# Performance work log

Measured on AMD Instinct MI355X. Metric: run time of the kernel, lower is better.

The kernel has to match this reference:

```python
import math
import jax, jax.numpy as jnp
import numpy as np

N_HEAD = 16

def setup_inputs() -> dict:
    key = jax.random.key(0)
    ks = jax.random.split(key, 7)
    B, T, C = 4, 2048, 1024
    QL, KVL = 256, 256
    s = 0.02
    return {
        "x":     jax.random.normal(ks[0], (B, T, C), jnp.float32),
        "W_dq":  jax.random.normal(ks[1], (QL, C), jnp.float32) * s,
        "W_uq":  jax.random.normal(ks[2], (C, QL), jnp.float32) * s,
        "W_dkv": jax.random.normal(ks[3], (KVL, C), jnp.float32) * s,
        "W_uk":  jax.random.normal(ks[4], (C, KVL), jnp.float32) * s,
        "W_uv":  jax.random.normal(ks[5], (C, KVL), jnp.float32) * s,
        "W_o":   jax.random.normal(ks[6], (C, C), jnp.float32) * s,
    }

def reference(x, W_dq, W_uq, W_dkv, W_uk, W_uv, W_o):
    B, T, C = x.shape
    nh = N_HEAD
    hs = C // nh
    kvl = W_dkv.shape[0]
    # Absorbed projection matrices (training path: recomputed each call)
    # k_eff: (nh, hs, kvl); v_eff: (nh, kvl, hs)
    k_eff = (W_dq.T @ W_uq.T @ W_uk).reshape(nh, hs, kvl)
    v_eff = (W_uv.T @ W_o.T).reshape(kvl, nh, hs).transpose(1, 0, 2)
    # Latent KV cache: (B, T, kvl)
    c_kv = x @ W_dkv.T
    # Queries: (B, nh, T, hs)
    q = (x @ W_dq.T @ W_uq.T).reshape(B, T, nh, hs).transpose(0, 2, 1, 3)
    # Scores: q @ k_eff @ c_kv^T / sqrt(hs) -> (B, nh, T, T)
    q_lat = jnp.einsum('bhtd,hdl->bhtl', q, k_eff)
    attn = jnp.einsum('bhtl,bsl->bhts', q_lat, c_kv) / math.sqrt(hs)
    causal_mask = jnp.triu(jnp.ones((T, T), bool), k=1)
    attn = jnp.where(causal_mask[None, None], -jnp.inf, attn)
    attn = jax.nn.softmax(attn, axis=-1)  # dropout p=0 -> identity
    # Output: attn @ c_kv @ v_eff -> (B, T, C)
    ctx = jnp.einsum('bhts,bsl->bhtl', attn, c_kv)
    y = jnp.einsum('bhtl,hld->bhtd', ctx, v_eff).transpose(0, 2, 1, 3).reshape(B, T, C)
    return (y, c_kv)
```

## Files before the change

### kernel.cpp

```cpp
#include <hip/hip_runtime.h>

typedef unsigned short u16;
typedef __attribute__((ext_vector_type(8))) short short8;
typedef __attribute__((ext_vector_type(4))) float f32x4;

#define MFMA_BF16 __builtin_amdgcn_mfma_f32_16x16x32_bf16

__device__ __forceinline__ u16 f2bf(float f){
  unsigned int u = __builtin_bit_cast(unsigned int, f);
  u += 0x7fffu + ((u >> 16) & 1u);
  return (u16)(u >> 16);
}

__device__ __forceinline__ void gld16(const void* g, void* l){
  __builtin_amdgcn_global_load_lds(
      (const __attribute__((address_space(1))) unsigned int*)g,
      (__attribute__((address_space(3))) unsigned int*)l, 16, 0, 0);
}

__global__ void k_transpose4(const float* __restrict__ s0, float* __restrict__ d0,
                             const float* __restrict__ s1, float* __restrict__ d1,
                             const float* __restrict__ s2, float* __restrict__ d2,
                             const float* __restrict__ s3, float* __restrict__ d3)
{
  __shared__ float tile[32][33];
  int z = blockIdx.z;
  const float* src = z == 0 ? s0 : z == 1 ? s1 : z == 2 ? s2 : s3;
  float* dst       = z == 0 ? d0 : z == 1 ? d1 : z == 2 ? d2 : d3;
  int rows = z == 0 ? 256 : 1024, cols = z == 0 ? 1024 : 256;
  int c0 = blockIdx.x * 32, r0 = blockIdx.y * 32;
  if (c0 >= cols || r0 >= rows) return;
  int tx = threadIdx.x, ty = threadIdx.y;
#pragma unroll
  for (int i = 0; i < 4; ++i){
    int r = ty + i * 8;
    tile[r][tx] = src[(long)(r0 + r) * cols + c0 + tx];
  }
  __syncthreads();
#pragma unroll
  for (int i = 0; i < 4; ++i){
    int r = ty + i * 8;
    dst[(long)(c0 + r) * rows + r0 + tx] = tile[tx][r];
  }
}

__global__ __launch_bounds__(256)
void k_gemm_nt(const float* __restrict__ A, const float* __restrict__ B,
               float* __restrict__ Cf, u16* __restrict__ Cb,
               int M, int N, int K, int lda, int ldb, int ldc,
               long sA, long sB, long sC, float scale)
{
  A += (long)blockIdx.z * sA; B += (long)blockIdx.z * sB;
  if (Cf) Cf += (long)blockIdx.z * sC;
  if (Cb) Cb += (long)blockIdx.z * sC;
  const int n0 = blockIdx.x * 64, m0 = blockIdx.y * 64;
  const int tid = threadIdx.x;
  const int wave = tid >> 6, lane = tid & 63, quad = lane >> 4, l16 = lane & 15;
  __shared__ u16 As[64 * 40];
  __shared__ u16 Bs[64 * 40];
  f32x4 acc[4];
#pragma unroll
  for (int n = 0; n < 4; ++n) acc[n] = (f32x4){0.f, 0.f, 0.f, 0.f};

  const int lr = tid >> 2;
  const int lc = (tid & 3) * 8;
  for (int k0 = 0; k0 < K; k0 += 32){
    {
      const float* pa = &A[(long)(m0 + lr) * lda + k0 + lc];
      float4 a0 = *(const float4*)pa;
      float4 a1 = *(const float4*)(pa + 4);
      short8 pk;
      pk[0]=(short)f2bf(a0.x); pk[1]=(short)f2bf(a0.y); pk[2]=(short)f2bf(a0.z); pk[3]=(short)f2bf(a0.w);
      pk[4]=(short)f2bf(a1.x); pk[5]=(short)f2bf(a1.y); pk[6]=(short)f2bf(a1.z); pk[7]=(short)f2bf(a1.w);
      *(short8*)&As[lr * 40 + lc] = pk;
      const float* pb = &B[(long)(n0 + lr) * ldb + k0 + lc];
      float4 b0 = *(const float4*)pb;
      float4 b1 = *(const float4*)(pb + 4);
      short8 qk;
      qk[0]=(short)f2bf(b0.x); qk[1]=(short)f2bf(b0.y); qk[2]=(short)f2bf(b0.z); qk[3]=(short)f2bf(b0.w);
      qk[4]=(short)f2bf(b1.x); qk[5]=(short)f2bf(b1.y); qk[6]=(short)f2bf(b1.z); qk[7]=(short)f2bf(b1.w);
      *(short8*)&Bs[lr * 40 + lc] = qk;
    }
    __syncthreads();
    short8 a = *(const short8*)&As[(wave * 16 + l16) * 40 + quad * 8];
#pragma unroll
    for (int n = 0; n < 4; ++n){
      short8 b = *(const short8*)&Bs[(n * 16 + l16) * 40 + quad * 8];
      acc[n] = MFMA_BF16(a, b, acc[n], 0, 0, 0);
    }
    __syncthreads();
  }
#pragma unroll
  for (int n = 0; n < 4; ++n)
#pragma unroll
    for (int r = 0; r < 4; ++r){
      int row = m0 + wave * 16 + quad * 4 + r;
      int col = n0 + n * 16 + l16;
      float v = acc[n][r] * scale;
      if (Cf) Cf[(long)row * ldc + col] = v;
      if (Cb) Cb[(long)row * ldc + col] = f2bf(v);
    }
}

__global__ __launch_bounds__(256)
void k_proj(const float* __restrict__ x, const float* __restrict__ Wdq,
            const float* __restrict__ Wdkv, u16* __restrict__ xq,
            float* __restrict__ ckv_f, u16* __restrict__ ckv_bf, u16* __restrict__ ckvT)
{
  const bool is_kv = blockIdx.x >= 4;
  const float* B = is_kv ? Wdkv : Wdq;
  const int n0 = (blockIdx.x & 3) * 64, m0 = blockIdx.y * 64;
  const int tid = threadIdx.x;
  const int wave = tid >> 6, lane = tid & 63, quad = lane >> 4, l16 = lane & 15;
  __shared__ u16 As[64 * 40];
  __shared__ u16 Bs[64 * 40];
  f32x4 acc[4];
#pragma unroll
  for (int n = 0; n < 4; ++n) acc[n] = (f32x4){0.f, 0.f, 0.f, 0.f};

  const int lr = tid >> 2;
  const int lc = (tid & 3) * 8;
  for (int k0 = 0; k0 < 1024; k0 += 32){
    {
      const float* pa = &x[(long)(m0 + lr) * 1024 + k0 + lc];
      float4 a0 = *(const float4*)pa;
      float4 a1 = *(const float4*)(pa + 4);
      short8 pk;
      pk[0]=(short)f2bf(a0.x); pk[1]=(short)f2bf(a0.y); pk[2]=(short)f2bf(a0.z); pk[3]=(short)f2bf(a0.w);
      pk[4]=(short)f2bf(a1.x); pk[5]=(short)f2bf(a1.y); pk[6]=(short)f2bf(a1.z); pk[7]=(short)f2bf(a1.w);
      *(short8*)&As[lr * 40 + lc] = pk;
      const float* pb = &B[(long)(n0 + lr) * 1024 + k0 + lc];
      float4 b0 = *(const float4*)pb;
      float4 b1 = *(const float4*)(pb + 4);
      short8 qk;
      qk[0]=(short)f2bf(b0.x); qk[1]=(short)f2bf(b0.y); qk[2]=(short)f2bf(b0.z); qk[3]=(short)f2bf(b0.w);
      qk[4]=(short)f2bf(b1.x); qk[5]=(short)f2bf(b1.y); qk[6]=(short)f2bf(b1.z); qk[7]=(short)f2bf(b1.w);
      *(short8*)&Bs[lr * 40 + lc] = qk;
    }
    __syncthreads();
    short8 a = *(const short8*)&As[(wave * 16 + l16) * 40 + quad * 8];
#pragma unroll
    for (int n = 0; n < 4; ++n){
      short8 b = *(const short8*)&Bs[(n * 16 + l16) * 40 + quad * 8];
      acc[n] = MFMA_BF16(a, b, acc[n], 0, 0, 0);
    }
    __syncthreads();
  }
  if (!is_kv){
#pragma unroll
    for (int n = 0; n < 4; ++n)
#pragma unroll
      for (int r = 0; r < 4; ++r){
        int row = m0 + wave * 16 + quad * 4 + r;
        int col = n0 + n * 16 + l16;
        xq[(long)row * 256 + col] = f2bf(acc[n][r]);
      }
  } else {
    const int b = (m0 >> 11);
    const int t0 = (m0 & 2047) + wave * 16 + quad * 4;
#pragma unroll
    for (int n = 0; n < 4; ++n){
      int col = n0 + n * 16 + l16;
      u16 pk[4];
#pragma unroll
      for (int r = 0; r < 4; ++r){
        int row = m0 + wave * 16 + quad * 4 + r;
        float v = acc[n][r];
        ckv_f [(long)row * 256 + col] = v;
        ckv_bf[(long)row * 256 + col] = f2bf(v);
        pk[r] = f2bf(v);
      }
      *(uint2*)&ckvT[((long)b * 256 + col) * 2048 + t0] = *(uint2*)pk;
    }
  }
}

__global__ __launch_bounds__(256, 2)
void k_flash(const u16* __restrict__ xq, const u16* __restrict__ Pt,
             const u16* __restrict__ ckv_bf, const u16* __restrict__ ckvT,
             const u16* __restrict__ Vt, float* __restrict__ y)
{
  const int qt = 31 - blockIdx.x, h = blockIdx.y, b = blockIdx.z;
  const int tid = threadIdx.x;
  const int wg = tid >> 6, lane = tid & 63, quad = lane >> 4, l16 = lane & 15;

  __shared__ u16 X0[64 * 256];
  __shared__ u16 X1[256 * 64];

  const int trow = wg * 16 + l16;
  const long tglob = (long)b * 2048 + qt * 64;
  const int sw_t = trow & 7;

  const u16* ckv_b  = ckv_bf + (long)b * 2048 * 256;
  const u16* ckvT_b = ckvT   + (long)b * 256 * 2048;

  const u16* srcA[8]; const u16* srcB[8];
  {
    int l5 = lane >> 5, g32 = lane & 31;
#pragma unroll
    for (int j = 0; j < 8; ++j){
      int s = (wg * 8 + j) * 2 + l5;
      int g = g32 ^ (s & 7);
      srcA[j] = ckv_b + (long)s * 256 + g * 8;
    }
    int l3 = lane >> 3, g8 = lane & 7;
#pragma unroll
    for (int j = 0; j < 8; ++j){
      int l = (wg * 8 + j) * 8 + l3;
      int g = g8 ^ (l & 7);
      srcB[j] = ckvT_b + (long)l * 2048 + g * 8;
    }
  }

  short8 aS[8];
  {
    short8 bq[8];
    const u16* xr = xq + (tglob + trow) * 256;
#pragma unroll
    for (int ks = 0; ks < 8; ++ks)
      bq[ks] = *(const short8*)&xr[ks * 32 + quad * 8];
    const u16* pth = Pt + (long)h * 65536;
#pragma unroll
    for (int mb = 0; mb < 16; ++mb){
      f32x4 acc = (f32x4){0.f, 0.f, 0.f, 0.f};
#pragma unroll
      for (int ks = 0; ks < 8; ++ks){
        short8 pa = *(const short8*)&pth[(mb * 16 + l16) * 256 + ks * 32 + quad * 8];
        acc = MFMA_BF16(pa, bq[ks], acc, 0, 0, 0);
      }
#pragma unroll
      for (int r = 0; r < 4; ++r){
        int l = mb * 16 + quad * 4 + r;
        int cs = (((l >> 3) ^ (l16 & 7)) << 3) | (l & 7);
        X0[trow * 256 + cs] = f2bf(acc[r]);
      }
    }
  }
  __syncthreads();
#pragma unroll
  for (int ks = 0; ks < 8; ++ks){
    int gl = ks * 4 + quad;
    aS[ks] = *(const short8*)&X0[trow * 256 + ((gl ^ sw_t) << 3)];
  }

  float m_t = -1e30f, l_t = 0.f;
  f32x4 oacc[16];
#pragma unroll
  for (int n = 0; n < 16; ++n) oacc[n] = (f32x4){0.f, 0.f, 0.f, 0.f};

  for (int st = 0; st <= qt; ++st){
    __syncthreads();
#pragma unroll
    for (int j = 0; j < 8; ++j)
      gld16(srcA[j] + (long)st * 16384, &X0[(wg * 8 + j) * 512]);
#pragma unroll
    for (int j = 0; j < 8; ++j)
      gld16(srcB[j] + st * 64, &X1[(wg * 8 + j) * 512]);
    __syncthreads();

    f32x4 sacc[4];
#pragma unroll
    for (int mb = 0; mb < 4; ++mb) sacc[mb] = (f32x4){0.f, 0.f, 0.f, 0.f};
#pragma unroll
    for (int ks = 0; ks < 8; ++ks){
#pragma unroll
      for (int mb = 0; mb < 4; ++mb){
        int gl = ks * 4 + quad;
        short8 a = *(const short8*)&X0[(mb * 16 + l16) * 256 + ((gl ^ (l16 & 7)) << 3)];
        sacc[mb] = MFMA_BF16(a, aS[ks], sacc[mb], 0, 0, 0);
      }
    }
    if (st == qt){
      int t = qt * 64 + trow;
#pragma unroll
      for (int mb = 0; mb < 4; ++mb)
#pragma unroll
        for (int r = 0; r < 4; ++r)
          if (st * 64 + mb * 16 + quad * 4 + r > t) sacc[mb][r] = -1e30f;
    }

    float pm[4][4];
    {
      float rm = sacc[0][0];
#pragma unroll
      for (int mb = 0; mb < 4; ++mb)
#pragma unroll
        for (int r = 0; r < 4; ++r) rm = fmaxf(rm, sacc[mb][r]);
      rm = fmaxf(rm, __shfl_xor(rm, 16, 64));
      rm = fmaxf(rm, __shfl_xor(rm, 32, 64));
      float mnew = fmaxf(m_t, rm);
      float alpha = __expf(m_t - mnew);
      m_t = mnew;
      float rs = 0.f;
#pragma unroll
      for (int mb = 0; mb < 4; ++mb)
#pragma unroll
        for (int r = 0; r < 4; ++r){
          float pe = __expf(sacc[mb][r] - mnew);
          pm[mb][r] = pe;
          rs += pe;
        }
      rs += __shfl_xor(rs, 16, 64);
      rs += __shfl_xor(rs, 32, 64);
      l_t = l_t * alpha + rs;
#pragma unroll
      for (int r2 = 0; r2 < 4; ++r2){
        float ar = __shfl(alpha, quad * 4 + r2, 64);
#pragma unroll
        for (int n = 0; n < 16; ++n) oacc[n][r2] *= ar;
      }
    }
    __syncthreads();
#pragma unroll
    for (int mb = 0; mb < 4; ++mb)
#pragma unroll
      for (int r = 0; r < 4; ++r)
        X0[trow * 72 + mb * 16 + quad * 4 + r] = f2bf(pm[mb][r]);
    __syncthreads();

    {
      short8 a0 = *(const short8*)&X0[trow * 72 + quad * 8];
      short8 a1 = *(const short8*)&X0[trow * 72 + 32 + quad * 8];
#pragma unroll
      for (int n = 0; n < 16; ++n){
        int lr_ = n * 16 + l16;
        int swl = lr_ & 7;
        short8 b0 = *(const short8*)&X1[lr_ * 64 + ((quad ^ swl) << 3)];
        short8 b1 = *(const short8*)&X1[lr_ * 64 + (((4 + quad) ^ swl) << 3)];
        oacc[n] = MFMA_BF16(a0, b0, oacc[n], 0, 0, 0);
        oacc[n] = MFMA_BF16(a1, b1, oacc[n], 0, 0, 0);
      }
    }
  }

  __syncthreads();
  {
    float linv = 1.f / l_t;
#pragma unroll
    for (int r = 0; r < 4; ++r){
      float lr_ = __shfl(linv, quad * 4 + r, 64);
#pragma unroll
      for (int n = 0; n < 16; ++n) oacc[n][r] *= lr_;
    }
#pragma unroll
    for (int n = 0; n < 16; ++n)
#pragma unroll
      for (int r = 0; r < 4; ++r){
        int trw = wg * 16 + quad * 4 + r;
        int l = n * 16 + l16;
        int cs = (((l >> 3) ^ (trw & 7)) << 3) | (l & 7);
        X0[trw * 256 + cs] = f2bf(oacc[n][r]);
      }
  }
  __syncthreads();
  {
    const u16* vth = Vt + (long)h * 64 * 256;
    short8 ca[8];
#pragma unroll
    for (int ks = 0; ks < 8; ++ks){
      int gl = ks * 4 + quad;
      ca[ks] = *(const short8*)&X0[trow * 256 + ((gl ^ sw_t) << 3)];
    }
#pragma unroll
    for (int n = 0; n < 4; ++n){
      f32x4 acc = (f32x4){0.f, 0.f, 0.f, 0.f};
#pragma unroll
      for (int ks = 0; ks < 8; ++ks){
        short8 vb = *(const short8*)&vth[(n * 16 + l16) * 256 + ks * 32 + quad * 8];
        acc = MFMA_BF16(ca[ks], vb, acc, 0, 0, 0);
      }
#pragma unroll
      for (int r = 0; r < 4; ++r)
        y[(tglob + wg * 16 + quad * 4 + r) * 1024 + h * 64 + n * 16 + l16] = acc[r];
    }
  }
}

extern "C" void kernel_launch(void* const* d_in, const int* in_sizes, int n_in,
                              void* d_out, int out_size, void* d_ws, size_t ws_size,
                              hipStream_t stream)
{
  (void)in_sizes; (void)n_in; (void)out_size; (void)ws_size;
  const float* x    = (const float*)d_in[0];
  const float* Wdq  = (const float*)d_in[1];
  const float* Wuq  = (const float*)d_in[2];
  const float* Wdkv = (const float*)d_in[3];
  const float* Wuk  = (const float*)d_in[4];
  const float* Wuv  = (const float*)d_in[5];
  const float* Wo   = (const float*)d_in[6];

  float* y_out   = (float*)d_out;
  float* ckv_out = y_out + (size_t)4 * 2048 * 1024;

  char* base = (char*)d_ws;
  float* wdqT   = (float*)(base + 0);
  float* wuqT   = (float*)(base + 1048576);
  float* wukT   = (float*)(base + 2097152);
  float* wuvT   = (float*)(base + 3145728);
  u16*   ckvT   = (u16*)  (base + 0);
  float* t1T    = (float*)(base + 4194304);
  float* keffT  = (float*)(base + 4456448);
  u16*   pt     = (u16*)  (base + 5505024);
  u16*   vt     = (u16*)  (base + 7602176);
  u16*   xq     = (u16*)  (base + 8126464);
  u16*   ckv_bf = (u16*)  (base + 12320768);

  k_transpose4<<<dim3(32, 32, 4), dim3(32, 8), 0, stream>>>(
      Wdq, wdqT, Wuq, wuqT, Wuk, wukT, Wuv, wuvT);

  k_gemm_nt<<<dim3(4, 4, 1), 256, 0, stream>>>(wukT, wuqT, t1T, (u16*)0,
      256, 256, 1024, 1024, 1024, 256, 0, 0, 0, 1.f);
  k_gemm_nt<<<dim3(16, 4, 1), 256, 0, stream>>>(t1T, wdqT, keffT, (u16*)0,
      256, 1024, 256, 256, 256, 1024, 0, 0, 0, 1.f);
  k_gemm_nt<<<dim3(4, 4, 16), 256, 0, stream>>>(keffT, wuqT, (float*)0, pt,
      256, 256, 64, 1024, 1024, 256, 64, 64, 65536, 0.125f);
  k_gemm_nt<<<dim3(4, 16, 1), 256, 0, stream>>>(Wo, wuvT, (float*)0, vt,
      1024, 256, 1024, 1024, 1024, 256, 0, 0, 0, 1.f);

  k_proj<<<dim3(8, 128), 256, 0, stream>>>(x, Wdq, Wdkv, xq, ckv_out, ckv_bf, ckvT);

  k_flash<<<dim3(32, 16, 4), 256, 0, stream>>>(xq, pt, ckv_bf, ckvT, vt, y_out);
}
```

Baseline: 737.9 us.

## Use 128-row query tiles with 8 waves and per-wave P buffers in flash kernel

Each flash block now covers 128 query rows with 512 threads (8 waves), so every loaded 64-key tile of the latent KV is shared by twice as many rows, halving global/LDS load traffic per row. The probability tile is written to a per-wave LDS buffer, which removes two block-wide barriers per iteration. Softmax rescaling is skipped unless the running max rises by more than 8 (lazy rescale), and MFMA sections get raised wave priority. Waves whose rows lie entirely before a key tile skip its compute but still join the loads. The trade-offs are more registers and LDS per block, and some imbalance between waves near the causal diagonal.

Result: slower. 795.7 us (+7.8%).

```diff
diff --git a/kernel.cpp b/kernel.cpp
--- a/kernel.cpp
+++ b/kernel.cpp
@@ -175,40 +175,40 @@
   }
 }
 
-__global__ __launch_bounds__(256, 2)
+__global__ __launch_bounds__(512, 4)
 void k_flash(const u16* __restrict__ xq, const u16* __restrict__ Pt,
              const u16* __restrict__ ckv_bf, const u16* __restrict__ ckvT,
              const u16* __restrict__ Vt, float* __restrict__ y)
 {
-  const int qt = 31 - blockIdx.x, h = blockIdx.y, b = blockIdx.z;
+  const int qt = 15 - blockIdx.x, h = blockIdx.y, b = blockIdx.z;
   const int tid = threadIdx.x;
   const int wg = tid >> 6, lane = tid & 63, quad = lane >> 4, l16 = lane & 15;
 
-  __shared__ u16 X0[64 * 256];
-  __shared__ u16 X1[256 * 64];
+  __shared__ u16 LDS[40960];
+  u16* X0 = LDS;
+  u16* X1 = LDS + 16384;
+  u16* PW = LDS + 32768 + wg * 1024;
 
   const int trow = wg * 16 + l16;
-  const long tglob = (long)b * 2048 + qt * 64;
-  const int sw_t = trow & 7;
+  const int swr  = l16 & 7;
+  const long tglob = (long)b * 2048 + qt * 128;
 
   const u16* ckv_b  = ckv_bf + (long)b * 2048 * 256;
   const u16* ckvT_b = ckvT   + (long)b * 256 * 2048;
 
-  const u16* srcA[8]; const u16* srcB[8];
+  int offA[4], offB[4];
   {
     int l5 = lane >> 5, g32 = lane & 31;
 #pragma unroll
-    for (int j = 0; j < 8; ++j){
-      int s = (wg * 8 + j) * 2 + l5;
-      int g = g32 ^ (s & 7);
-      srcA[j] = ckv_b + (long)s * 256 + g * 8;
+    for (int j = 0; j < 4; ++j){
+      int s = (wg * 4 + j) * 2 + l5;
+      offA[j] = s * 256 + ((g32 ^ (s & 7)) * 8);
     }
     int l3 = lane >> 3, g8 = lane & 7;
 #pragma unroll
-    for (int j = 0; j < 8; ++j){
-      int l = (wg * 8 + j) * 8 + l3;
-      int g = g8 ^ (l & 7);
-      srcB[j] = ckvT_b + (long)l * 2048 + g * 8;
+    for (int j = 0; j < 4; ++j){
+      int l = (wg * 4 + j) * 8 + l3;
+      offB[j] = l * 2048 + ((g8 ^ (l & 7)) * 8);
     }
   }
 
@@ -231,8 +231,8 @@
 #pragma unroll
       for (int r = 0; r < 4; ++r){
         int l = mb * 16 + quad * 4 + r;
-        int cs = (((l >> 3) ^ (l16 & 7)) << 3) | (l & 7);
-        X0[trow * 256 + cs] = f2bf(acc[r]);
+        int cs = (((l >> 3) ^ swr) << 3) | (l & 7);
+        LDS[trow * 256 + cs] = f2bf(acc[r]);
       }
     }
   }
@@ -240,7 +240,7 @@
 #pragma unroll
   for (int ks = 0; ks < 8; ++ks){
     int gl = ks * 4 + quad;
-    aS[ks] = *(const short8*)&X0[trow * 256 + ((gl ^ sw_t) << 3)];
+    aS[ks] = *(const short8*)&LDS[trow * 256 + ((gl ^ swr) << 3)];
   }
 
   float m_t = -1e30f, l_t = 0.f;
@@ -248,61 +248,55 @@
 #pragma unroll
   for (int n = 0; n < 16; ++n) oacc[n] = (f32x4){0.f, 0.f, 0.f, 0.f};
 
-  for (int st = 0; st <= qt; ++st){
-    __syncthreads();
-#pragma unroll
-    for (int j = 0; j < 8; ++j)
-      gld16(srcA[j] + (long)st * 16384, &X0[(wg * 8 + j) * 512]);
-#pragma unroll
-    for (int j = 0; j < 8; ++j)
-      gld16(srcB[j] + st * 64, &X1[(wg * 8 + j) * 512]);
-    __syncthreads();
+  const int stmax = 2 * qt + 1;
+  const int tg = qt * 128 + trow;
+  for (int st = 0; st <= stmax; ++st){
+    __syncthreads();
+#pragma unroll
+    for (int j = 0; j < 4; ++j)
+      gld16(ckv_b + (long)st * 16384 + offA[j], &X0[(wg * 4 + j) * 512]);
+#pragma unroll
+    for (int j = 0; j < 4; ++j)
+      gld16(ckvT_b + st * 64 + offB[j], &X1[(wg * 4 + j) * 512]);
+    __syncthreads();
+
+    if (st * 64 > qt * 128 + wg * 16 + 15) continue;
 
     f32x4 sacc[4];
 #pragma unroll
     for (int mb = 0; mb < 4; ++mb) sacc[mb] = (f32x4){0.f, 0.f, 0.f, 0.f};
+    __builtin_amdgcn_s_setprio(1);
 #pragma unroll
     for (int ks = 0; ks < 8; ++ks){
+      int gl = ks * 4 + quad;
 #pragma unroll
       for (int mb = 0; mb < 4; ++mb){
-        int gl = ks * 4 + quad;
-        short8 a = *(const short8*)&X0[(mb * 16 + l16) * 256 + ((gl ^ (l16 & 7)) << 3)];
+        short8 a = *(const short8*)&X0[(mb * 16 + l16) * 256 + ((gl ^ swr) << 3)];
         sacc[mb] = MFMA_BF16(a, aS[ks], sacc[mb], 0, 0, 0);
       }
     }
-    if (st == qt){
-      int t = qt * 64 + trow;
+    __builtin_amdgcn_s_setprio(0);
+
+    if (st * 64 + 63 > tg){
 #pragma unroll
       for (int mb = 0; mb < 4; ++mb)
 #pragma unroll
         for (int r = 0; r < 4; ++r)
-          if (st * 64 + mb * 16 + quad * 4 + r > t) sacc[mb][r] = -1e30f;
-    }
-
-    float pm[4][4];
-    {
-      float rm = sacc[0][0];
-#pragma unroll
-      for (int mb = 0; mb < 4; ++mb)
-#pragma unroll
-        for (int r = 0; r < 4; ++r) rm = fmaxf(rm, sacc[mb][r]);
-      rm = fmaxf(rm, __shfl_xor(rm, 16, 64));
-      rm = fmaxf(rm, __shfl_xor(rm, 32, 64));
+          if (st * 64 + mb * 16 + quad * 4 + r > tg) sacc[mb][r] = -1e30f;
+    }
+
+    float rm = sacc[0][0];
+#pragma unroll
+    for (int mb = 0; mb < 4; ++mb)
+#pragma unroll
+      for (int r = 0; r < 4; ++r) rm = fmaxf(rm, sacc[mb][r]);
+    rm = fmaxf(rm, __shfl_xor(rm, 16, 64));
+    rm = fmaxf(rm, __shfl_xor(rm, 32, 64));
+    if (!__all(rm <= m_t + 8.f)){
       float mnew = fmaxf(m_t, rm);
       float alpha = __expf(m_t - mnew);
       m_t = mnew;
-      float rs = 0.f;
-#pragma unroll
-      for (int mb = 0; mb < 4; ++mb)
-#pragma unroll
-        for (int r = 0; r < 4; ++r){
-          float pe = __expf(sacc[mb][r] - mnew);
-          pm[mb][r] = pe;
-          rs += pe;
-        }
-      rs += __shfl_xor(rs, 16, 64);
-      rs += __shfl_xor(rs, 32, 64);
-      l_t = l_t * alpha + rs;
+      l_t *= alpha;
 #pragma unroll
       for (int r2 = 0; r2 < 4; ++r2){
         float ar = __shfl(alpha, quad * 4 + r2, 64);
@@ -310,27 +304,37 @@
         for (int n = 0; n < 16; ++n) oacc[n][r2] *= ar;
       }
     }
-    __syncthreads();
-#pragma unroll
-    for (int mb = 0; mb < 4; ++mb)
-#pragma unroll
-      for (int r = 0; r < 4; ++r)
-        X0[trow * 72 + mb * 16 + quad * 4 + r] = f2bf(pm[mb][r]);
-    __syncthreads();
-
-    {
-      short8 a0 = *(const short8*)&X0[trow * 72 + quad * 8];
-      short8 a1 = *(const short8*)&X0[trow * 72 + 32 + quad * 8];
-#pragma unroll
-      for (int n = 0; n < 16; ++n){
-        int lr_ = n * 16 + l16;
-        int swl = lr_ & 7;
-        short8 b0 = *(const short8*)&X1[lr_ * 64 + ((quad ^ swl) << 3)];
-        short8 b1 = *(const short8*)&X1[lr_ * 64 + (((4 + quad) ^ swl) << 3)];
-        oacc[n] = MFMA_BF16(a0, b0, oacc[n], 0, 0, 0);
-        oacc[n] = MFMA_BF16(a1, b1, oacc[n], 0, 0, 0);
-      }
-    }
+    float rs = 0.f;
+#pragma unroll
+    for (int mb = 0; mb < 4; ++mb){
+      float p0 = __expf(sacc[mb][0] - m_t);
+      float p1 = __expf(sacc[mb][1] - m_t);
+      float p2 = __expf(sacc[mb][2] - m_t);
+      float p3 = __expf(sacc[mb][3] - m_t);
+      rs += (p0 + p1) + (p2 + p3);
+      unsigned int w0 = (unsigned)f2bf(p0) | ((unsigned)f2bf(p1) << 16);
+      unsigned int w1 = (unsigned)f2bf(p2) | ((unsigned)f2bf(p3) << 16);
+      int pos = (2 * mb + (quad >> 1)) ^ swr;
+      uint2 w; w.x = w0; w.y = w1;
+      *(uint2*)&PW[l16 * 64 + pos * 8 + (quad & 1) * 4] = w;
+    }
+    rs += __shfl_xor(rs, 16, 64);
+    rs += __shfl_xor(rs, 32, 64);
+    l_t += rs;
+
+    short8 a0 = *(const short8*)&PW[l16 * 64 + ((quad ^ swr) << 3)];
+    short8 a1 = *(const short8*)&PW[l16 * 64 + (((4 + quad) ^ swr) << 3)];
+    __builtin_amdgcn_s_setprio(1);
+#pragma unroll
+    for (int n = 0; n < 16; ++n){
+      int lr_ = n * 16 + l16;
+      int swl = lr_ & 7;
+      short8 b0 = *(const short8*)&X1[lr_ * 64 + ((quad ^ swl) << 3)];
+      short8 b1 = *(const short8*)&X1[lr_ * 64 + (((4 + quad) ^ swl) << 3)];
+      oacc[n] = MFMA_BF16(a0, b0, oacc[n], 0, 0, 0);
+      oacc[n] = MFMA_BF16(a1, b1, oacc[n], 0, 0, 0);
+    }
+    __builtin_amdgcn_s_setprio(0);
   }
 
   __syncthreads();
@@ -349,7 +353,7 @@
         int trw = wg * 16 + quad * 4 + r;
         int l = n * 16 + l16;
         int cs = (((l >> 3) ^ (trw & 7)) << 3) | (l & 7);
-        X0[trw * 256 + cs] = f2bf(oacc[n][r]);
+        LDS[trw * 256 + cs] = f2bf(oacc[n][r]);
       }
   }
   __syncthreads();
@@ -359,7 +363,7 @@
 #pragma unroll
     for (int ks = 0; ks < 8; ++ks){
       int gl = ks * 4 + quad;
-      ca[ks] = *(const short8*)&X0[trow * 256 + ((gl ^ sw_t) << 3)];
+      ca[ks] = *(const short8*)&LDS[trow * 256 + ((gl ^ swr) << 3)];
     }
 #pragma unroll
     for (int n = 0; n < 4; ++n){
@@ -419,5 +423,5 @@
 
   k_proj<<<dim3(8, 128), 256, 0, stream>>>(x, Wdq, Wdkv, xq, ckv_out, ckv_bf, ckvT);
 
-  k_flash<<<dim3(32, 16, 4), 256, 0, stream>>>(xq, pt, ckv_bf, ckvT, vt, y_out);
-}
+  k_flash<<<dim3(16, 16, 4), 512, 0, stream>>>(xq, pt, ckv_bf, ckvT, vt, y_out);
+}
```
